# Optimization experiments

Hardware: AMD Instinct MI355X
Metric: run time of the kernel (lower is better)

## Reference

```python
import jax, jax.numpy as jnp
import numpy as np
from jax import lax

D = 33            # n_vertices
NEG_SLOPE = 0.2   # LeakyReLU slope
EPS_IN = 1e-5     # InstanceNorm eps


def _block(x, w, b, gamma, beta):
    # Conv2d(k=3, stride=2, pad=1) -> LeakyReLU(0.2) -> optional InstanceNorm2d(affine)
    y = lax.conv_general_dilated(x, w, (2, 2), [(1, 1), (1, 1)],
                                 dimension_numbers=('NCHW', 'OIHW', 'NCHW'))
    y = y + b[None, :, None, None]
    y = jnp.where(y >= 0, y, NEG_SLOPE * y)
    if gamma is not None:
        mu = jnp.mean(y, (2, 3), keepdims=True)
        var = jnp.var(y, (2, 3), keepdims=True)
        y = (y - mu) * lax.rsqrt(var + EPS_IN) * gamma[None, :, None, None] + beta[None, :, None, None]
    return y


def _backbone(lq, w1, b1, g1, be1, w2, b2, g2, be2, w3, b3, g3, be3,
              w4, b4, g4, be4, w5, b5):
    B = lq.shape[0]
    # F.interpolate(..., 256, bilinear, align_corners=False) == half-pixel linear, no antialias
    x = jax.image.resize(lq, (B, 3, 256, 256), method='linear', antialias=False)
    x = _block(x, w1, b1, g1, be1)   # [B,16,128,128]
    x = _block(x, w2, b2, g2, be2)   # [B,32,64,64]
    x = _block(x, w3, b3, g3, be3)   # [B,64,32,32]
    x = _block(x, w4, b4, g4, be4)   # [B,128,16,16]
    x = _block(x, w5, b5, None, None)  # [B,128,8,8]; Dropout is identity in eval
    # AdaptiveAvgPool2d(2) on 8x8 -> mean over 4x4 blocks
    x = x.reshape(B, 128, 2, 4, 2, 4).mean((3, 5))  # [B,128,2,2]
    return x.reshape(B, -1)  # [B,512]


def _trilerp(lut, r, g, b):
    # lut [3,D,D,D]; r,g,b [N] in [0, D-1]; align_corners=True + border padding
    i0 = jnp.clip(jnp.floor(r).astype(jnp.int32), 0, D - 2)
    j0 = jnp.clip(jnp.floor(g).astype(jnp.int32), 0, D - 2)
    k0 = jnp.clip(jnp.floor(b).astype(jnp.int32), 0, D - 2)
    fr, fg, fb = r - i0, g - j0, b - k0

    def c(di, dj, dk):
        return lut[:, i0 + di, j0 + dj, k0 + dk]  # [3,N]

    return (c(0, 0, 0) * (1 - fr) * (1 - fg) * (1 - fb)
            + c(0, 0, 1) * (1 - fr) * (1 - fg) * fb
            + c(0, 1, 0) * (1 - fr) * fg * (1 - fb)
            + c(0, 1, 1) * (1 - fr) * fg * fb
            + c(1, 0, 0) * fr * (1 - fg) * (1 - fb)
            + c(1, 0, 1) * fr * (1 - fg) * fb
            + c(1, 1, 0) * fr * fg * (1 - fb)
            + c(1, 1, 1) * fr * fg * fb)


def _ailut_transform(img, luts, vertices):
    # img [B,3,H,W] in [0,1]; luts [B,3,D,D,D]; vertices [B,3,D] sorted in [0,1]
    B, C, H, W = img.shape
    p = img.reshape(B, C, -1)  # [B,3,N]
    # per-(b,c) searchsorted(right=True)
    idx = jax.vmap(jax.vmap(lambda v, x: jnp.searchsorted(v, x, side='right')))(vertices, p)
    idx = jnp.clip(idx, 1, D - 1)
    v_lo = jnp.take_along_axis(vertices, idx - 1, axis=-1)
    v_hi = jnp.take_along_axis(vertices, idx, axis=-1)
    frac = (p - v_lo) / (v_hi - v_lo + 1e-8)
    coord = (idx - 1).astype(img.dtype) + frac        # [B,3,N] in [0, D-1]
    coord = jnp.clip(coord, 0.0, D - 1.0)             # border padding
    # torch grid layout (blue->W, green->H, red->D); LUT axes are (red, green, blue)
    sampled = jax.vmap(_trilerp)(luts, coord[:, 0], coord[:, 1], coord[:, 2])  # [B,3,N]
    return sampled.reshape(B, C, H, W)


def _forward(lq, w1, b1, g1, be1, w2, b2, g2, be2, w3, b3, g3, be3,
             w4, b4, g4, be4, w5, b5, lw, lb, bw, aw, ab):
    B = lq.shape[0]
    codes = _backbone(lq, w1, b1, g1, be1, w2, b2, g2, be2, w3, b3, g3, be3,
                      w4, b4, g4, be4, w5, b5)          # [B,512]
    # LUTGenerator
    weights = codes @ lw.T + lb                          # [B,3]
    luts = (weights @ bw.T).reshape(B, 3, D, D, D)       # [B,3,D,D,D]
    # AdaInt
    intervals = (codes @ aw.T + ab).reshape(B, 3, D - 1)
    intervals = jax.nn.softmax(intervals, axis=-1)
    vertices = jnp.pad(jnp.cumsum(intervals, axis=-1), ((0, 0), (0, 0), (1, 0)))  # [B,3,D]
    outs = jnp.clip(_ailut_transform(lq, luts, vertices), 0.0, 1.0)
    return outs, weights, vertices


def setup_inputs() -> dict:
    key = jax.random.key(0)
    ks = jax.random.split(key, 16)
    B = 4
    lq = jax.random.uniform(ks[0], (B, 3, 1024, 1024), jnp.float32)

    def cw(k, o, i):
        return jax.random.normal(k, (o, i, 3, 3), jnp.float32) * (1.0 / np.sqrt(i * 9))

    w1 = cw(ks[1], 16, 3);   b1 = jnp.zeros(16);  g1 = jnp.ones(16);  be1 = jnp.zeros(16)
    w2 = cw(ks[2], 32, 16);  b2 = jnp.zeros(32);  g2 = jnp.ones(32);  be2 = jnp.zeros(32)
    w3 = cw(ks[3], 64, 32);  b3 = jnp.zeros(64);  g3 = jnp.ones(64);  be3 = jnp.zeros(64)
    w4 = cw(ks[4], 128, 64); b4 = jnp.zeros(128); g4 = jnp.ones(128); be4 = jnp.zeros(128)
    w5 = cw(ks[5], 128, 128); b5 = jnp.zeros(128)

    lw = jax.random.normal(ks[6], (3, 512), jnp.float32) * 0.02
    lb = jnp.ones(3, jnp.float32)  # init: bias = ones
    # basis LUT bank: rank0 = identity LUT (meshgrid/(D-1), channel-flipped), others small
    grid = jnp.stack(jnp.meshgrid(jnp.arange(D), jnp.arange(D), jnp.arange(D),
                                  indexing='ij'), 0).astype(jnp.float32) / (D - 1)
    identity = grid[::-1].reshape(-1, 1)  # [3*D^3,1]
    bw = jnp.concatenate([identity,
                          jax.random.normal(ks[7], (3 * D ** 3, 2), jnp.float32) * 0.01], axis=1)
    aw = jax.random.normal(ks[8], (96, 512), jnp.float32) * 0.01
    ab = jnp.ones(96, jnp.float32)  # init: bias = ones
    return {'lq': lq, 'w1': w1, 'b1': b1, 'g1': g1, 'be1': be1,
            'w2': w2, 'b2': b2, 'g2': g2, 'be2': be2,
            'w3': w3, 'b3': b3, 'g3': g3, 'be3': be3,
            'w4': w4, 'b4': b4, 'g4': g4, 'be4': be4,
            'w5': w5, 'b5': b5, 'lw': lw, 'lb': lb, 'bw': bw, 'aw': aw, 'ab': ab}


def reference(lq, w1, b1, g1, be1, w2, b2, g2, be2, w3, b3, g3, be3,
              w4, b4, g4, be4, w5, b5, lw, lb, bw, aw, ab):
    return _forward(lq, w1, b1, g1, be1, w2, b2, g2, be2, w3, b3, g3, be3,
                    w4, b4, g4, be4, w5, b5, lw, lb, bw, aw, ab)
```

## Files before the change

kernel.cpp:

```cpp
#include <hip/hip_runtime.h>
#include <hip/hip_fp16.h>
#include <math.h>

#define LUT_D 33
#define LUT_D3 35937
#define NEG 0.2f
#define BATCH 4
#define HW_IMG 1048576

__global__ void k_resize(const float* __restrict__ lq, float* __restrict__ out) {
    int gid = blockIdx.x * 256 + threadIdx.x;
    if (gid >= BATCH * 3 * 256 * 256) return;
    int x  = gid & 255;
    int y  = (gid >> 8) & 255;
    int pc = gid >> 16;
    const float* in = lq + (size_t)pc * HW_IMG;
    const float* p0 = in + (4 * y + 1) * 1024 + (4 * x + 1);
    out[gid] = 0.25f * (p0[0] + p0[1] + p0[1024] + p0[1025]);
}

template<int IC, int OC, int OH, int OW, int NSPLIT, bool NORM_IN, bool STATS_OUT>
__global__ void __launch_bounds__(256) k_conv_t(
    const float* __restrict__ in, const float* __restrict__ nrm_in,
    const float* __restrict__ w, const float* __restrict__ bias,
    float* __restrict__ out, float* __restrict__ part) {
    constexpr int IH = OH * 2, IW = OW * 2;
    constexpr int ICB = IC / NSPLIT;
    constexpr int TROW = 20, TSZ = 17 * TROW;
    constexpr int WQ = ICB * 9 / 4;
    constexpr int NTX = OW / 8, NTY = OH / 8, NOCG = OC / 16;
    constexpr int NT = NTX * NTY;
    constexpr int PX = OH * OW;

    __shared__ float sIn[ICB * TSZ];
    __shared__ float swl[16 * ICB * 9];
    __shared__ float sNm[NORM_IN ? ICB * 2 : 1];

    int id = blockIdx.x;
    int ocg   = id % NOCG;   id /= NOCG;
    int icc_i = id % NSPLIT; id /= NSPLIT;
    int tx    = id % NTX;    id /= NTX;
    int ty    = id % NTY;    id /= NTY;
    int b     = id;
    int icc   = icc_i * ICB;

    int t    = threadIdx.x;
    int lane = t >> 6;
    int px   = t & 63;
    int py   = px >> 3, pxx = px & 7;
    int oc0  = ocg * 16 + lane * 4;

    if (IC == ICB) {
        const float4* wsrc = (const float4*)(w + (size_t)ocg * 16 * IC * 9);
        for (int i = t; i < 16 * IC * 9 / 4; i += 256) ((float4*)swl)[i] = wsrc[i];
    } else {
        for (int i = t; i < 16 * WQ; i += 256) {
            int ol = i / WQ, qi = i % WQ;
            ((float4*)swl)[ol * WQ + qi] =
                *(const float4*)(w + ((size_t)(ocg * 16 + ol) * IC + icc) * 9 + qi * 4);
        }
    }
    if (NORM_IN) {
        for (int i = t; i < ICB * 2; i += 256) sNm[i] = nrm_in[(b * IC + icc) * 2 + i];
    }
    __syncthreads();

    int iy0 = ty * 16 - 1;
    int xbase = tx * 16;
    const float* inb = in + (size_t)(b * IC + icc) * (IH * IW);
    for (int q = t; q < ICB * 17 * 4; q += 256) {
        int ic_l = q / 68;
        int r    = q % 68;
        int row  = r >> 2, quad = r & 3;
        int iy = iy0 + row;
        float4 v = {0.f, 0.f, 0.f, 0.f};
        if (iy >= 0 && iy < IH) {
            v = *(const float4*)(inb + (size_t)ic_l * (IH * IW) + (size_t)iy * IW + xbase + quad * 4);
            if (NORM_IN) {
                float sc = sNm[ic_l * 2], sh = sNm[ic_l * 2 + 1];
                v.x = v.x * sc + sh; v.y = v.y * sc + sh;
                v.z = v.z * sc + sh; v.w = v.w * sc + sh;
            }
        }
        *(float4*)(sIn + ic_l * TSZ + row * TROW + 4 + quad * 4) = v;
    }
    for (int h = t; h < ICB * 17; h += 256) {
        int ic_l = h / 17, row = h % 17;
        int iy = iy0 + row, ix = xbase - 1;
        float v = 0.f;
        if (iy >= 0 && iy < IH && ix >= 0) {
            v = inb[(size_t)ic_l * (IH * IW) + (size_t)iy * IW + ix];
            if (NORM_IN) v = v * sNm[ic_l * 2] + sNm[ic_l * 2 + 1];
        }
        sIn[ic_l * TSZ + row * TROW + 3] = v;
    }
    __syncthreads();

    float acc[4];
    #pragma unroll
    for (int j = 0; j < 4; j++) acc[j] = (NSPLIT == 1) ? bias[oc0 + j] : 0.f;

    for (int i2 = 0; i2 < ICB; i2++) {
        const float* tp = sIn + i2 * TSZ + py * 2 * TROW + pxx * 2 + 3;
        float x0 = tp[0],        x1 = tp[1],        x2 = tp[2];
        float x3 = tp[TROW],     x4 = tp[TROW + 1], x5 = tp[TROW + 2];
        float x6 = tp[2 * TROW], x7 = tp[2 * TROW + 1], x8 = tp[2 * TROW + 2];
        #pragma unroll
        for (int j = 0; j < 4; j++) {
            const float* wp = swl + ((lane * 4 + j) * ICB + i2) * 9;
            acc[j] = fmaf(x0, wp[0], acc[j]);
            acc[j] = fmaf(x1, wp[1], acc[j]);
            acc[j] = fmaf(x2, wp[2], acc[j]);
            acc[j] = fmaf(x3, wp[3], acc[j]);
            acc[j] = fmaf(x4, wp[4], acc[j]);
            acc[j] = fmaf(x5, wp[5], acc[j]);
            acc[j] = fmaf(x6, wp[6], acc[j]);
            acc[j] = fmaf(x7, wp[7], acc[j]);
            acc[j] = fmaf(x8, wp[8], acc[j]);
        }
    }

    int oy = ty * 8 + py, ox = tx * 8 + pxx;
    if (NSPLIT == 1) {
        int tile = ty * NTX + tx;
        #pragma unroll
        for (int j = 0; j < 4; j++) {
            float a = acc[j];
            a = a >= 0.f ? a : NEG * a;
            out[((size_t)(b * OC + oc0 + j) * OH + oy) * OW + ox] = a;
            if (STATS_OUT) {
                float s1 = a, s2 = a * a;
                for (int off = 32; off > 0; off >>= 1) {
                    s1 += __shfl_down(s1, off, 64);
                    s2 += __shfl_down(s2, off, 64);
                }
                if (px == 0) {
                    size_t pi = ((size_t)(b * OC + oc0 + j) * NT + tile) * 2;
                    part[pi] = s1; part[pi + 1] = s2;
                }
            }
        }
    } else {
        #pragma unroll
        for (int j = 0; j < 4; j++) {
            part[(size_t)icc_i * (BATCH * OC * PX) +
                 (size_t)(b * OC + oc0 + j) * PX + oy * OW + ox] = acc[j];
        }
    }
}

template<int NSPLIT, int OC, int PX, bool STATS>
__global__ void k_combine(const float* __restrict__ ps, const float* __restrict__ bias,
                          float* __restrict__ out, float* __restrict__ spart) {
    constexpr int TOT = BATCH * OC * PX;
    int e = blockIdx.x * 256 + threadIdx.x;
    if (e >= TOT) return;
    float s = 0.f;
    #pragma unroll
    for (int k = 0; k < NSPLIT; k++) s += ps[(size_t)k * TOT + e];
    int oc = (e / PX) % OC;
    s += bias[oc];
    s = s >= 0.f ? s : NEG * s;
    out[e] = s;
    if (STATS) {
        float s1 = s, s2 = s * s;
        for (int off = 32; off > 0; off >>= 1) {
            s1 += __shfl_down(s1, off, 64);
            s2 += __shfl_down(s2, off, 64);
        }
        if ((threadIdx.x & 63) == 0) {
            int widx = e >> 6;
            spart[widx * 2] = s1; spart[widx * 2 + 1] = s2;
        }
    }
}

template<int NT>
__global__ void k_norm(const float* __restrict__ part, const float* __restrict__ g,
                       const float* __restrict__ be, float invN, int C,
                       float* __restrict__ nrm) {
    int bc = blockIdx.x;
    int t  = threadIdx.x;
    float s1 = 0.f, s2 = 0.f;
    for (int i = t; i < NT; i += 64) {
        s1 += part[((size_t)bc * NT + i) * 2];
        s2 += part[((size_t)bc * NT + i) * 2 + 1];
    }
    #pragma unroll
    for (int off = 32; off > 0; off >>= 1) {
        s1 += __shfl_down(s1, off, 64);
        s2 += __shfl_down(s2, off, 64);
    }
    if (t == 0) {
        int c = bc % C;
        float m   = s1 * invN;
        float var = s2 * invN - m * m;
        float sc  = g[c] * rsqrtf(var + 1e-5f);
        nrm[bc * 2]     = sc;
        nrm[bc * 2 + 1] = be[c] - m * sc;
    }
}

__global__ void k_pool(const float* __restrict__ f5, float* __restrict__ codes) {
    int c = blockIdx.x * 256 + threadIdx.x;
    if (c >= 2048) return;
    int b = c >> 9;
    int rest = c & 511;
    int oc = rest >> 2, q = rest & 3;
    int py = (q >> 1) * 4, px = (q & 1) * 4;
    const float* p = f5 + ((size_t)(b * 128 + oc)) * 64;
    float s = 0.f;
    #pragma unroll
    for (int dy = 0; dy < 4; dy++)
        #pragma unroll
        for (int dx = 0; dx < 4; dx++)
            s += p[(py + dy) * 8 + px + dx];
    codes[c] = s * (1.f / 16.f);
}

__global__ void k_head(const float* __restrict__ codes, const float* __restrict__ lw,
                       const float* __restrict__ lb, const float* __restrict__ aw,
                       const float* __restrict__ ab, float* __restrict__ wt,
                       float* __restrict__ vert, float* __restrict__ stab,
                       float* __restrict__ out_w, float* __restrict__ out_v) {
    int blk = blockIdx.x;
    int t = threadIdx.x;
    if (blk == 12) {
        if (t < 12) {
            int b = t / 3, j = t % 3;
            const float* c = codes + b * 512;
            const float* l = lw + j * 512;
            float s = lb[j];
            for (int k = 0; k < 512; k++) s += c[k] * l[k];
            wt[t] = s;
            out_w[t] = s;
        }
        return;
    }
    int b = blk / 3, ch = blk % 3;
    __shared__ float y[32];
    __shared__ float vsh[33];
    if (t < 32) {
        const float* c = codes + b * 512;
        const float* a = aw + (size_t)(ch * 32 + t) * 512;
        float s = ab[ch * 32 + t];
        for (int k = 0; k < 512; k++) s += c[k] * a[k];
        y[t] = s;
    }
    __syncthreads();
    if (t == 0) {
        float mx = y[0];
        for (int m = 1; m < 32; m++) mx = fmaxf(mx, y[m]);
        float e[32];
        float sum = 0.f;
        for (int m = 0; m < 32; m++) { e[m] = expf(y[m] - mx); sum += e[m]; }
        float inv = 1.f / sum;
        float cum = 0.f;
        float* vb = vert + (b * 3 + ch) * 33;
        float* ob = out_v + (b * 3 + ch) * 33;
        vb[0] = 0.f; ob[0] = 0.f; vsh[0] = 0.f;
        for (int m = 0; m < 32; m++) {
            cum += e[m] * inv;
            vb[m + 1] = cum; ob[m + 1] = cum; vsh[m + 1] = cum;
        }
    }
    __syncthreads();
    unsigned char* sb = (unsigned char*)stab + (b * 3 + ch) * 256;
    for (int u = t; u < 256; u += 64) {
        float lo = (float)u * (1.f / 256.f);
        int cnt = 0;
        #pragma unroll
        for (int m = 0; m < 33; m++) cnt += (vsh[m] <= lo) ? 1 : 0;
        sb[u] = (unsigned char)cnt;
    }
}

__global__ void k_lutgen(const float* __restrict__ bw, const float* __restrict__ wt,
                         float4* __restrict__ lutp) {
    int gid = blockIdx.x * 256 + threadIdx.x;
    if (gid >= BATCH * LUT_D3) return;
    int b = gid / LUT_D3;
    int cell = gid - b * LUT_D3;
    int k = cell % LUT_D;
    int cn = (k < LUT_D - 1) ? cell + 1 : cell;
    float w0 = wt[b * 3], w1 = wt[b * 3 + 1], w2 = wt[b * 3 + 2];
    const float* r0p = bw + (size_t)(0 * LUT_D3 + cell) * 3;
    const float* g0p = bw + (size_t)(1 * LUT_D3 + cell) * 3;
    const float* b0p = bw + (size_t)(2 * LUT_D3 + cell) * 3;
    const float* r1p = bw + (size_t)(0 * LUT_D3 + cn) * 3;
    const float* g1p = bw + (size_t)(1 * LUT_D3 + cn) * 3;
    const float* b1p = bw + (size_t)(2 * LUT_D3 + cn) * 3;
    union { float4 f4; __half h[8]; } u;
    u.h[0] = __float2half_rn(r0p[0] * w0 + r0p[1] * w1 + r0p[2] * w2);
    u.h[1] = __float2half_rn(g0p[0] * w0 + g0p[1] * w1 + g0p[2] * w2);
    u.h[2] = __float2half_rn(b0p[0] * w0 + b0p[1] * w1 + b0p[2] * w2);
    u.h[3] = __float2half_rn(r1p[0] * w0 + r1p[1] * w1 + r1p[2] * w2);
    u.h[4] = __float2half_rn(g1p[0] * w0 + g1p[1] * w1 + g1p[2] * w2);
    u.h[5] = __float2half_rn(b1p[0] * w0 + b1p[1] * w1 + b1p[2] * w2);
    u.h[6] = __float2half_rn(0.f);
    u.h[7] = __float2half_rn(0.f);
    lutp[gid] = u.f4;
}

__global__ void k_cellgen(const float4* __restrict__ lutp, float4* __restrict__ cells) {
    int gid = blockIdx.x * 256 + threadIdx.x;
    if (gid >= BATCH * 32768) return;
    int b = gid >> 15;
    int cell = gid & 32767;
    int k0 = cell & 31, j0 = (cell >> 5) & 31, i0 = cell >> 10;
    const float4* L = lutp + (size_t)b * LUT_D3;
    int base = (i0 * LUT_D + j0) * LUT_D + k0;
    float4 e00 = L[base];
    float4 e01 = L[base + LUT_D];
    float4 e10 = L[base + LUT_D * LUT_D];
    float4 e11 = L[base + LUT_D * LUT_D + LUT_D];
    float4 o0, o1, o2;
    o0.x = e00.x; o0.y = e00.y; o0.z = e00.z;
    o0.w = e01.x; o1.x = e01.y; o1.y = e01.z;
    o1.z = e10.x; o1.w = e10.y; o2.x = e10.z;
    o2.y = e11.x; o2.z = e11.y; o2.w = e11.z;
    float4* dst = cells + (size_t)gid * 4;
    dst[0] = o0; dst[1] = o1; dst[2] = o2;
}

__device__ __forceinline__ void searchA(const float* __restrict__ v,
                                        const unsigned char* __restrict__ tab,
                                        float x, int& i0, float& f) {
    int u = (int)(x * 256.f);
    u = u < 0 ? 0 : (u > 255 ? 255 : u);
    int idx = tab[u];
    while (idx < LUT_D && v[idx] <= x) idx++;
    idx = idx < 1 ? 1 : (idx > LUT_D - 1 ? LUT_D - 1 : idx);
    float vl = v[idx - 1], vh = v[idx];
    float fr = (x - vl) / (vh - vl + 1e-8f);
    float coord = (float)(idx - 1) + fr;
    coord = fminf(fmaxf(coord, 0.f), (float)(LUT_D - 1));
    i0 = (int)coord;
    if (i0 > LUT_D - 2) i0 = LUT_D - 2;
    f = coord - (float)i0;
}

__device__ __forceinline__ void decode_lerp3(float wa, float wb, float wc, float fb,
                                             float& rv, float& gv, float& bv) {
    union { float f; __half2 h; } u0, u1, u2;
    u0.f = wa; u1.f = wb; u2.f = wc;
    float2 a = __half22float2(u0.h);
    float2 b = __half22float2(u1.h);
    float2 c = __half22float2(u2.h);
    rv = fmaf(fb, b.y - a.x, a.x);
    gv = fmaf(fb, c.x - a.y, a.y);
    bv = fmaf(fb, c.y - b.x, b.x);
}

__global__ void __launch_bounds__(256) k_transform(const float* __restrict__ lq,
                                                   const float4* __restrict__ cells,
                                                   const float* __restrict__ vert,
                                                   const unsigned char* __restrict__ stab,
                                                   float* __restrict__ out) {
    int bimg = blockIdx.x >> 10;
    int blk  = blockIdx.x & 1023;
    __shared__ float sv[3 * LUT_D];
    __shared__ unsigned char st[768];
    if (threadIdx.x < 3 * LUT_D) sv[threadIdx.x] = vert[bimg * 3 * LUT_D + threadIdx.x];
    if (threadIdx.x < 192)
        ((unsigned int*)st)[threadIdx.x] = ((const unsigned int*)stab)[bimg * 192 + threadIdx.x];
    __syncthreads();
    int p0 = blk * 1024 + threadIdx.x * 4;
    const float* lr = lq + (size_t)bimg * 3 * HW_IMG + p0;
    float4 r4 = *(const float4*)(lr);
    float4 g4 = *(const float4*)(lr + HW_IMG);
    float4 b4 = *(const float4*)(lr + 2 * HW_IMG);
    float rr[4] = {r4.x, r4.y, r4.z, r4.w};
    float gg[4] = {g4.x, g4.y, g4.z, g4.w};
    float bb[4] = {b4.x, b4.y, b4.z, b4.w};

    int cidx[4];
    float fra[4], fga[4], fba[4];
    #pragma unroll
    for (int i = 0; i < 4; i++) {
        int i0, j0, k0;
        searchA(sv,      st,       rr[i], i0, fra[i]);
        searchA(sv + 33, st + 256, gg[i], j0, fga[i]);
        searchA(sv + 66, st + 512, bb[i], k0, fba[i]);
        cidx[i] = ((i0 * 32 + j0) << 5) + k0;
    }
    float4 c0[4], c1[4], c2[4];
    #pragma unroll
    for (int i = 0; i < 4; i++) {
        const float4* p = cells + (((size_t)(bimg << 15) + cidx[i]) << 2);
        c0[i] = p[0]; c1[i] = p[1]; c2[i] = p[2];
    }
    float ro[4], go[4], bo[4];
    #pragma unroll
    for (int i = 0; i < 4; i++) {
        float fb = fba[i];
        float r00, g00, b00, r01, g01, b01, r10, g10, b10, r11, g11, b11;
        decode_lerp3(c0[i].x, c0[i].y, c0[i].z, fb, r00, g00, b00);
        decode_lerp3(c0[i].w, c1[i].x, c1[i].y, fb, r01, g01, b01);
        decode_lerp3(c1[i].z, c1[i].w, c2[i].x, fb, r10, g10, b10);
        decode_lerp3(c2[i].y, c2[i].z, c2[i].w, fb, r11, g11, b11);
        float fr = fra[i], fg = fga[i];
        float w00 = (1.f - fr) * (1.f - fg), w01 = (1.f - fr) * fg;
        float w10 = fr * (1.f - fg),         w11 = fr * fg;
        float rx = r00 * w00 + r01 * w01 + r10 * w10 + r11 * w11;
        float ry = g00 * w00 + g01 * w01 + g10 * w10 + g11 * w11;
        float rz = b00 * w00 + b01 * w01 + b10 * w10 + b11 * w11;
        ro[i] = fminf(fmaxf(rx, 0.f), 1.f);
        go[i] = fminf(fmaxf(ry, 0.f), 1.f);
        bo[i] = fminf(fmaxf(rz, 0.f), 1.f);
    }
    float* op = out + (size_t)bimg * 3 * HW_IMG + p0;
    float4 o0 = {ro[0], ro[1], ro[2], ro[3]};
    float4 o1 = {go[0], go[1], go[2], go[3]};
    float4 o2 = {bo[0], bo[1], bo[2], bo[3]};
    *(float4*)(op) = o0;
    *(float4*)(op + HW_IMG) = o1;
    *(float4*)(op + 2 * HW_IMG) = o2;
}

extern "C" void kernel_launch(void* const* d_in, const int* in_sizes, int n_in,
                              void* d_out, int out_size, void* d_ws, size_t ws_size,
                              hipStream_t stream) {
    const float* lq  = (const float*)d_in[0];
    const float* w1  = (const float*)d_in[1];
    const float* b1  = (const float*)d_in[2];
    const float* g1  = (const float*)d_in[3];
    const float* be1 = (const float*)d_in[4];
    const float* w2  = (const float*)d_in[5];
    const float* b2  = (const float*)d_in[6];
    const float* g2  = (const float*)d_in[7];
    const float* be2 = (const float*)d_in[8];
    const float* w3  = (const float*)d_in[9];
    const float* b3  = (const float*)d_in[10];
    const float* g3  = (const float*)d_in[11];
    const float* be3 = (const float*)d_in[12];
    const float* w4  = (const float*)d_in[13];
    const float* b4  = (const float*)d_in[14];
    const float* g4  = (const float*)d_in[15];
    const float* be4 = (const float*)d_in[16];
    const float* w5  = (const float*)d_in[17];
    const float* b5  = (const float*)d_in[18];
    const float* lw  = (const float*)d_in[19];
    const float* lb  = (const float*)d_in[20];
    const float* bw  = (const float*)d_in[21];
    const float* aw  = (const float*)d_in[22];
    const float* ab  = (const float*)d_in[23];

    float* ws     = (float*)d_ws;
    float* r256   = ws;
    float* f1     = r256 + 786432;
    float* f2     = f1 + 1048576;
    float* f3     = f2 + 524288;
    float* f4     = f3 + 262144;
    float* f5     = f4 + 131072;
    float* codes  = f5 + 32768;
    float* wt     = codes + 2048;
    float* vert   = wt + 12;
    float* part1  = vert + 396;
    float* part2  = part1 + 32768;
    float* part3  = part2 + 16384;
    float* spart4 = part3 + 8192;
    float* norm1  = spart4 + 4096;
    float* norm2  = norm1 + 128;
    float* norm3  = norm2 + 256;
    float* norm4  = norm3 + 512;
    float* stab   = norm4 + 1024;
    float* luts4  = stab + 768;
    float* psplit4 = f1;
    float* psplit5 = f1 + 262144;
    float* cells  = ws;

    float* outs  = (float*)d_out;
    float* out_w = outs + (size_t)BATCH * 3 * HW_IMG;
    float* out_v = out_w + 12;

    k_resize<<<3072, 256, 0, stream>>>(lq, r256);
    k_conv_t<3, 16, 128, 128, 1, false, true><<<1024, 256, 0, stream>>>(
        r256, nullptr, w1, b1, f1, part1);
    k_norm<256><<<64, 64, 0, stream>>>(part1, g1, be1, 1.f / 16384.f, 16, norm1);
    k_conv_t<16, 32, 64, 64, 1, true, true><<<512, 256, 0, stream>>>(
        f1, norm1, w2, b2, f2, part2);
    k_norm<64><<<128, 64, 0, stream>>>(part2, g2, be2, 1.f / 4096.f, 32, norm2);
    k_conv_t<32, 64, 32, 32, 1, true, true><<<256, 256, 0, stream>>>(
        f2, norm2, w3, b3, f3, part3);
    k_norm<16><<<256, 64, 0, stream>>>(part3, g3, be3, 1.f / 1024.f, 64, norm3);
    k_conv_t<64, 128, 16, 16, 2, true, false><<<256, 256, 0, stream>>>(
        f3, norm3, w4, b4, nullptr, psplit4);
    k_combine<2, 128, 256, true><<<512, 256, 0, stream>>>(psplit4, b4, f4, spart4);
    k_norm<4><<<512, 64, 0, stream>>>(spart4, g4, be4, 1.f / 256.f, 128, norm4);
    k_conv_t<128, 128, 8, 8, 4, true, false><<<128, 256, 0, stream>>>(
        f4, norm4, w5, b5, nullptr, psplit5);
    k_combine<4, 128, 64, false><<<128, 256, 0, stream>>>(psplit5, b5, f5, nullptr);
    k_pool<<<8, 256, 0, stream>>>(f5, codes);
    k_head<<<13, 64, 0, stream>>>(codes, lw, lb, aw, ab, wt, vert, stab, out_w, out_v);
    k_lutgen<<<(BATCH * LUT_D3 + 255) / 256, 256, 0, stream>>>(bw, wt, (float4*)luts4);
    k_cellgen<<<512, 256, 0, stream>>>((const float4*)luts4, (float4*)cells);
    k_transform<<<BATCH * 1024, 256, 0, stream>>>(
        lq, (const float4*)cells, vert, (const unsigned char*)stab, outs);
}
```

Measured before the change: 291.8 us.

## Precompute per-bin linear coordinate tables, vectorize resize and head, deepen conv splits

The per-pixel vertex search in the transform kernel is replaced by a 256-bin table holding slope and intercept pairs, so each channel lookup becomes one FMA. A binary-search fallback handles bins that contain two or more vertices. The resize kernel now uses float4 loads and produces four outputs per thread, the head matvecs use vectorized loads with shuffle reductions, and conv4 and conv5 use larger input-channel splits to launch more blocks. In exchange the transform kernel loads more shared memory per block, and the partial-sum buffers and combine kernels grow.

```diff
diff --git a/kernel.cpp b/kernel.cpp
--- a/kernel.cpp
+++ b/kernel.cpp
@@ -10,13 +10,21 @@
 
 __global__ void k_resize(const float* __restrict__ lq, float* __restrict__ out) {
     int gid = blockIdx.x * 256 + threadIdx.x;
-    if (gid >= BATCH * 3 * 256 * 256) return;
-    int x  = gid & 255;
-    int y  = (gid >> 8) & 255;
-    int pc = gid >> 16;
-    const float* in = lq + (size_t)pc * HW_IMG;
-    const float* p0 = in + (4 * y + 1) * 1024 + (4 * x + 1);
-    out[gid] = 0.25f * (p0[0] + p0[1] + p0[1024] + p0[1025]);
+    if (gid >= BATCH * 3 * 256 * 64) return;
+    int xq = gid & 63;
+    int y  = (gid >> 6) & 255;
+    int pc = gid >> 14;
+    const float* ra = lq + (size_t)pc * HW_IMG + (size_t)(4 * y + 1) * 1024 + xq * 16;
+    const float4* pa = (const float4*)ra;
+    const float4* pb = (const float4*)(ra + 1024);
+    float4 a0 = pa[0], a1 = pa[1], a2 = pa[2], a3 = pa[3];
+    float4 b0 = pb[0], b1 = pb[1], b2 = pb[2], b3 = pb[3];
+    float4 o;
+    o.x = 0.25f * (a0.y + a0.z + b0.y + b0.z);
+    o.y = 0.25f * (a1.y + a1.z + b1.y + b1.z);
+    o.z = 0.25f * (a2.y + a2.z + b2.y + b2.z);
+    o.w = 0.25f * (a3.y + a3.z + b3.y + b3.z);
+    ((float4*)out)[gid] = o;
 }
 
 template<int IC, int OC, int OH, int OW, int NSPLIT, bool NORM_IN, bool STATS_OUT>
@@ -221,31 +229,46 @@
 __global__ void k_head(const float* __restrict__ codes, const float* __restrict__ lw,
                        const float* __restrict__ lb, const float* __restrict__ aw,
                        const float* __restrict__ ab, float* __restrict__ wt,
-                       float* __restrict__ vert, float* __restrict__ stab,
-                       float* __restrict__ out_w, float* __restrict__ out_v) {
+                       float* __restrict__ vert, float* __restrict__ tabA,
+                       float* __restrict__ tabC, float* __restrict__ out_w,
+                       float* __restrict__ out_v) {
     int blk = blockIdx.x;
     int t = threadIdx.x;
     if (blk == 12) {
-        if (t < 12) {
-            int b = t / 3, j = t % 3;
-            const float* c = codes + b * 512;
-            const float* l = lw + j * 512;
-            float s = lb[j];
-            for (int k = 0; k < 512; k++) s += c[k] * l[k];
-            wt[t] = s;
-            out_w[t] = s;
+        if (t < 48) {
+            int j = t >> 2, q = t & 3;
+            int b = j / 3, jj = j % 3;
+            const float4* c4 = (const float4*)(codes + b * 512 + q * 128);
+            const float4* l4 = (const float4*)(lw + jj * 512 + q * 128);
+            float s = 0.f;
+            for (int k = 0; k < 32; k++) {
+                float4 cv = c4[k], lv = l4[k];
+                s += cv.x * lv.x + cv.y * lv.y + cv.z * lv.z + cv.w * lv.w;
+            }
+            s += __shfl_down(s, 2, 64);
+            s += __shfl_down(s, 1, 64);
+            if (q == 0) {
+                s += lb[jj];
+                wt[j] = s;
+                out_w[j] = s;
+            }
         }
         return;
     }
     int b = blk / 3, ch = blk % 3;
     __shared__ float y[32];
     __shared__ float vsh[33];
-    if (t < 32) {
-        const float* c = codes + b * 512;
-        const float* a = aw + (size_t)(ch * 32 + t) * 512;
-        float s = ab[ch * 32 + t];
-        for (int k = 0; k < 512; k++) s += c[k] * a[k];
-        y[t] = s;
+    {
+        int m = t & 31, half = t >> 5;
+        const float4* c4 = (const float4*)(codes + b * 512 + half * 256);
+        const float4* a4 = (const float4*)(aw + (size_t)(ch * 32 + m) * 512 + half * 256);
+        float s = (half == 0) ? ab[ch * 32 + m] : 0.f;
+        for (int k = 0; k < 64; k++) {
+            float4 cv = c4[k], av = a4[k];
+            s += cv.x * av.x + cv.y * av.y + cv.z * av.z + cv.w * av.w;
+        }
+        s += __shfl_down(s, 32, 64);
+        if (half == 0) y[m] = s;
     }
     __syncthreads();
     if (t == 0) {
@@ -265,13 +288,28 @@
         }
     }
     __syncthreads();
-    unsigned char* sb = (unsigned char*)stab + (b * 3 + ch) * 256;
+    float4* A4 = ((float4*)tabA) + (b * 3 + ch) * 256;
+    float*  C1 = tabC + (b * 3 + ch) * 256;
     for (int u = t; u < 256; u += 64) {
         float lo = (float)u * (1.f / 256.f);
-        int cnt = 0;
+        float hi = (float)(u + 1) * (1.f / 256.f);
+        int n0 = 0, nin = 0;
+        float vs = 2.0f;
         #pragma unroll
-        for (int m = 0; m < 33; m++) cnt += (vsh[m] <= lo) ? 1 : 0;
-        sb[u] = (unsigned char)cnt;
+        for (int m = 0; m < 33; m++) {
+            float vm = vsh[m];
+            n0 += (vm <= lo) ? 1 : 0;
+            if (vm > lo && vm < hi) { if (nin == 0) vs = vm; nin++; }
+        }
+        int i0 = n0 < 1 ? 1 : (n0 > 32 ? 32 : n0);
+        int i1 = (n0 + 1) < 1 ? 1 : ((n0 + 1) > 32 ? 32 : (n0 + 1));
+        float m0 = 1.f / (vsh[i0] - vsh[i0 - 1] + 1e-8f);
+        float c0 = (float)(i0 - 1) - vsh[i0 - 1] * m0;
+        float m1 = 1.f / (vsh[i1] - vsh[i1 - 1] + 1e-8f);
+        float c1 = (float)(i1 - 1) - vsh[i1 - 1] * m1;
+        if (nin >= 2) { vs = 2.0f; m0 = __int_as_float(0x7fc00000); c0 = 0.f; }
+        A4[u] = make_float4(vs, m0, c0, m1);
+        C1[u] = c1;
     }
 }
 
@@ -323,17 +361,22 @@
     dst[0] = o0; dst[1] = o1; dst[2] = o2;
 }
 
-__device__ __forceinline__ void searchA(const float* __restrict__ v,
-                                        const unsigned char* __restrict__ tab,
+__device__ __forceinline__ void searchL(const float4* __restrict__ A,
+                                        const float* __restrict__ C,
+                                        const float* __restrict__ v33,
                                         float x, int& i0, float& f) {
     int u = (int)(x * 256.f);
     u = u < 0 ? 0 : (u > 255 ? 255 : u);
-    int idx = tab[u];
-    while (idx < LUT_D && v[idx] <= x) idx++;
-    idx = idx < 1 ? 1 : (idx > LUT_D - 1 ? LUT_D - 1 : idx);
-    float vl = v[idx - 1], vh = v[idx];
-    float fr = (x - vl) / (vh - vl + 1e-8f);
-    float coord = (float)(idx - 1) + fr;
+    float4 e = A[u];
+    float c1 = C[u];
+    float coord = (x < e.x) ? fmaf(e.y, x, e.z) : fmaf(e.w, x, c1);
+    if (!(coord == coord)) {
+        int lo = 0, hi = LUT_D;
+        while (lo < hi) { int mid = (lo + hi) >> 1; if (v33[mid] <= x) lo = mid + 1; else hi = mid; }
+        int idx = lo < 1 ? 1 : (lo > LUT_D - 1 ? LUT_D - 1 : lo);
+        float vl = v33[idx - 1], vh = v33[idx];
+        coord = (float)(idx - 1) + (x - vl) / (vh - vl + 1e-8f);
+    }
     coord = fminf(fmaxf(coord, 0.f), (float)(LUT_D - 1));
     i0 = (int)coord;
     if (i0 > LUT_D - 2) i0 = LUT_D - 2;
@@ -355,21 +398,28 @@
 __global__ void __launch_bounds__(256) k_transform(const float* __restrict__ lq,
                                                    const float4* __restrict__ cells,
                                                    const float* __restrict__ vert,
-                                                   const unsigned char* __restrict__ stab,
+                                                   const float* __restrict__ gA,
+                                                   const float* __restrict__ gC,
                                                    float* __restrict__ out) {
     int bimg = blockIdx.x >> 10;
     int blk  = blockIdx.x & 1023;
-    __shared__ float sv[3 * LUT_D];
-    __shared__ unsigned char st[768];
-    if (threadIdx.x < 3 * LUT_D) sv[threadIdx.x] = vert[bimg * 3 * LUT_D + threadIdx.x];
-    if (threadIdx.x < 192)
-        ((unsigned int*)st)[threadIdx.x] = ((const unsigned int*)stab)[bimg * 192 + threadIdx.x];
-    __syncthreads();
+    __shared__ float4 sA[3 * 256];
+    __shared__ float  sC[3 * 256];
+    __shared__ float  sv[3 * LUT_D + 1];
+
     int p0 = blk * 1024 + threadIdx.x * 4;
     const float* lr = lq + (size_t)bimg * 3 * HW_IMG + p0;
     float4 r4 = *(const float4*)(lr);
     float4 g4 = *(const float4*)(lr + HW_IMG);
     float4 b4 = *(const float4*)(lr + 2 * HW_IMG);
+
+    const float4* gA4 = (const float4*)gA;
+    for (int i = threadIdx.x; i < 768; i += 256) sA[i] = gA4[bimg * 768 + i];
+    for (int i = threadIdx.x; i < 192; i += 256)
+        ((float4*)sC)[i] = ((const float4*)gC)[bimg * 192 + i];
+    if (threadIdx.x < 99) sv[threadIdx.x] = vert[bimg * 99 + threadIdx.x];
+    __syncthreads();
+
     float rr[4] = {r4.x, r4.y, r4.z, r4.w};
     float gg[4] = {g4.x, g4.y, g4.z, g4.w};
     float bb[4] = {b4.x, b4.y, b4.z, b4.w};
@@ -379,9 +429,9 @@
     #pragma unroll
     for (int i = 0; i < 4; i++) {
         int i0, j0, k0;
-        searchA(sv,      st,       rr[i], i0, fra[i]);
-        searchA(sv + 33, st + 256, gg[i], j0, fga[i]);
-        searchA(sv + 66, st + 512, bb[i], k0, fba[i]);
+        searchL(sA,       sC,       sv,      rr[i], i0, fra[i]);
+        searchL(sA + 256, sC + 256, sv + 33, gg[i], j0, fga[i]);
+        searchL(sA + 512, sC + 512, sv + 66, bb[i], k0, fba[i]);
         cidx[i] = ((i0 * 32 + j0) << 5) + k0;
     }
     float4 c0[4], c1[4], c2[4];
@@ -464,17 +514,18 @@
     float* norm2  = norm1 + 128;
     float* norm3  = norm2 + 256;
     float* norm4  = norm3 + 512;
-    float* stab   = norm4 + 1024;
-    float* luts4  = stab + 768;
+    float* tabA   = norm4 + 1024;
+    float* tabC   = tabA + 12288;
+    float* luts4  = tabC + 3072;
     float* psplit4 = f1;
-    float* psplit5 = f1 + 262144;
+    float* psplit5 = f1 + 524288;
     float* cells  = ws;
 
     float* outs  = (float*)d_out;
     float* out_w = outs + (size_t)BATCH * 3 * HW_IMG;
     float* out_v = out_w + 12;
 
-    k_resize<<<3072, 256, 0, stream>>>(lq, r256);
+    k_resize<<<768, 256, 0, stream>>>(lq, r256);
     k_conv_t<3, 16, 128, 128, 1, false, true><<<1024, 256, 0, stream>>>(
         r256, nullptr, w1, b1, f1, part1);
     k_norm<256><<<64, 64, 0, stream>>>(part1, g1, be1, 1.f / 16384.f, 16, norm1);
@@ -484,17 +535,17 @@
     k_conv_t<32, 64, 32, 32, 1, true, true><<<256, 256, 0, stream>>>(
         f2, norm2, w3, b3, f3, part3);
     k_norm<16><<<256, 64, 0, stream>>>(part3, g3, be3, 1.f / 1024.f, 64, norm3);
-    k_conv_t<64, 128, 16, 16, 2, true, false><<<256, 256, 0, stream>>>(
+    k_conv_t<64, 128, 16, 16, 4, true, false><<<512, 256, 0, stream>>>(
         f3, norm3, w4, b4, nullptr, psplit4);
-    k_combine<2, 128, 256, true><<<512, 256, 0, stream>>>(psplit4, b4, f4, spart4);
+    k_combine<4, 128, 256, true><<<512, 256, 0, stream>>>(psplit4, b4, f4, spart4);
     k_norm<4><<<512, 64, 0, stream>>>(spart4, g4, be4, 1.f / 256.f, 128, norm4);
-    k_conv_t<128, 128, 8, 8, 4, true, false><<<128, 256, 0, stream>>>(
+    k_conv_t<128, 128, 8, 8, 8, true, false><<<256, 256, 0, stream>>>(
         f4, norm4, w5, b5, nullptr, psplit5);
-    k_combine<4, 128, 64, false><<<128, 256, 0, stream>>>(psplit5, b5, f5, nullptr);
+    k_combine<8, 128, 64, false><<<128, 256, 0, stream>>>(psplit5, b5, f5, nullptr);
     k_pool<<<8, 256, 0, stream>>>(f5, codes);
-    k_head<<<13, 64, 0, stream>>>(codes, lw, lb, aw, ab, wt, vert, stab, out_w, out_v);
+    k_head<<<13, 64, 0, stream>>>(codes, lw, lb, aw, ab, wt, vert, tabA, tabC, out_w, out_v);
     k_lutgen<<<(BATCH * LUT_D3 + 255) / 256, 256, 0, stream>>>(bw, wt, (float4*)luts4);
     k_cellgen<<<512, 256, 0, stream>>>((const float4*)luts4, (float4*)cells);
     k_transform<<<BATCH * 1024, 256, 0, stream>>>(
-        lq, (const float4*)cells, vert, (const unsigned char*)stab, outs);
-}
+        lq, (const float4*)cells, vert, tabA, tabC, outs);
+}
```

Result: faster. 284.3 us (-2.6%).
